# Performance work log

Measured on AMD Instinct MI355X. Metric: run time of the kernel, lower is better.

The kernel has to match this reference:

```python
import jax, jax.numpy as jnp
import numpy as np

B, D, M, R, C = 1024, 32, 8, 4096, 32
TOPK_P = 0.1  # hard-coded in torch forward
EPS = 1e-9


def setup_inputs() -> dict:
    key = jax.random.key(0)
    k0, k1, k2, k3, k4 = jax.random.split(key, 5)
    x = jax.random.normal(k0, (B, D), dtype=jnp.float32)
    centers = jax.random.normal(k1, (D, M), dtype=jnp.float32)
    # widths kept away from 0 so gaussian MFs don't all underflow
    widths = jax.random.uniform(k2, (D, M), dtype=jnp.float32, minval=0.5, maxval=1.5)
    consequents = jax.random.uniform(k3, (R, D + 1, C), dtype=jnp.float32)
    rules = jax.random.randint(k4, (R, D), 0, M, dtype=jnp.int32)
    return {"x": x, "centers": centers, "widths": widths,
            "consequents": consequents, "rules": rules}


def reference(x, centers, widths, consequents, rules):
    Bn, Dn = x.shape
    Rn = rules.shape[0]
    # Gaussian membership functions: (B, D, M)
    mfs = jnp.exp(-((x[:, :, None] - centers[None]) ** 2) / (2.0 * widths[None] ** 2))
    # Gather per-rule MF values: (B, D, R)  (torch.gather along mf axis)
    rule_mfs = mfs[:, jnp.arange(Dn)[:, None], rules.T]
    # Firing strengths via product over input dims: (B, R)
    firing = jnp.prod(rule_mfs, axis=1)
    # top-K gate + scatter mask
    K = max(1, int(TOPK_P * Rn))
    _, idx = jax.lax.top_k(firing, K)
    mask = jnp.zeros_like(firing).at[jnp.arange(Bn)[:, None], idx].set(1.0)
    firing = firing * mask
    norm_fs = firing / (firing.sum(axis=1, keepdims=True) + EPS)
    # zeroG=False branch. Torch does einsum('bi,rjc->brc', x_ext, consequents)
    # which sums i and j independently: rule_mfs[b,r,c] = sum_i(x_ext[b,i]) * sum_j(cons[r,j,c]).
    # Then einsum('br,brc->bc') => out = sum(x_ext,1) * (norm_fs @ sum(cons,1)).
    x_ext_sum = x.sum(axis=1) + 1.0          # sum over x_ext = [x, 1], shape (B,)
    cons_sum = consequents.sum(axis=1)       # (R, C)
    rule_outputs = x_ext_sum[:, None] * (norm_fs @ cons_sum)  # (B, C)
    return rule_outputs, norm_fs, mask
```

## Files before the change

kernel.cpp:

```cpp
#include <hip/hip_runtime.h>

#define Bn 1024
#define Dn 32
#define Mn 8
#define Rn 4096
#define Cn 32
#define Kn 409
#define NTH 512
#define NBIN 1024
#define CCAP 256

typedef unsigned int u32;
typedef unsigned short u16;
typedef short bf16x8 __attribute__((ext_vector_type(8)));
typedef float f32x4 __attribute__((ext_vector_type(4)));

__device__ __forceinline__ int binof(float kf) {
    int b = (int)floorf(kf * (float)(NBIN / 120.0) + (float)NBIN);
    return b < 0 ? 0 : (b > NBIN - 1 ? NBIN - 1 : b);
}

__device__ __forceinline__ u16 f2bf(float v) {
    u32 b = __float_as_uint(v);
    b += 0x7fffu + ((b >> 16) & 1u);
    return (u16)(b >> 16);
}

__device__ __forceinline__ uint4 onehot4(int v) {
    uint4 o;
    o.x = (v == 0 ? 0x3F80u : 0u) | (v == 1 ? (0x3F80u << 16) : 0u);
    o.y = (v == 2 ? 0x3F80u : 0u) | (v == 3 ? (0x3F80u << 16) : 0u);
    o.z = (v == 4 ? 0x3F80u : 0u) | (v == 5 ? (0x3F80u << 16) : 0u);
    o.w = (v == 6 ? 0x3F80u : 0u) | (v == 7 ? (0x3F80u << 16) : 0u);
    return o;
}

__global__ __launch_bounds__(NTH, 8) void key_gemm_kernel(
    const float* __restrict__ x, const float* __restrict__ centers,
    const float* __restrict__ widths, const float* __restrict__ cons,
    const int* __restrict__ rules,
    float* __restrict__ cons_sum, float* __restrict__ keys)
{
    __shared__ float s_cen[256];
    __shared__ float s_inv[256];
    __shared__ u16 sAh[32 * 32];
    __shared__ u16 sAl[32 * 32];
    __shared__ u16 sB[128 * 32];

    const int blk = blockIdx.x;
    const int t = threadIdx.x;
    const int lane = t & 63;
    const int w = t >> 6;
    const int m0 = (blk >> 5) * 32;
    const int n0 = (blk & 31) * 128;
    const int wr = w >> 2;
    const int wc = w & 3;

    if (t < 256) {
        const float ww = widths[t];
        s_cen[t] = centers[t];
        s_inv[t] = 0.5f / (ww * ww);
    }

    f32x4 acc0 = (f32x4){0.f, 0.f, 0.f, 0.f};
    f32x4 acc1 = (f32x4){0.f, 0.f, 0.f, 0.f};

    const int brow = t >> 2;
    const int aj = t & 3;
    const int cidx = blk * 128 + (t & 127);
    const float* cp = cons + (size_t)(cidx >> 5) * ((Dn + 1) * Cn) + (cidx & 31);
    float csum = 0.f;
    __syncthreads();

#pragma unroll
    for (int ki = 0; ki < 8; ++ki) {
        const int d0 = ki * 4;
        {
            const int v = rules[(size_t)(n0 + brow) * Dn + d0 + aj];
            *(uint4*)(sB + brow * 32 + aj * 8) = onehot4(v);
        }
        if (t < 128) {
            const int arow = t >> 2;
            const float xv = x[(size_t)(m0 + arow) * Dn + d0 + aj];
            const int dm0 = (d0 + aj) * 8;
            u16 h[8], l[8];
#pragma unroll
            for (int m = 0; m < 8; ++m) {
                const float dx = xv - s_cen[dm0 + m];
                const float e = -(dx * dx) * s_inv[dm0 + m];
                const u16 hb = f2bf(e);
                h[m] = hb;
                l[m] = f2bf(e - __uint_as_float((u32)hb << 16));
            }
            *(uint4*)(sAh + arow * 32 + aj * 8) =
                make_uint4((u32)h[0] | ((u32)h[1] << 16), (u32)h[2] | ((u32)h[3] << 16),
                           (u32)h[4] | ((u32)h[5] << 16), (u32)h[6] | ((u32)h[7] << 16));
            *(uint4*)(sAl + arow * 32 + aj * 8) =
                make_uint4((u32)l[0] | ((u32)l[1] << 16), (u32)l[2] | ((u32)l[3] << 16),
                           (u32)l[4] | ((u32)l[5] << 16), (u32)l[6] | ((u32)l[7] << 16));
#pragma unroll
            for (int q = 0; q < 4; ++q) csum += cp[(ki * 4 + q) * Cn];
        }
        __syncthreads();
        bf16x8 ah = *(const bf16x8*)(sAh + ((wr * 16 + (lane & 15)) * 32 + (lane >> 4) * 8));
        bf16x8 al = *(const bf16x8*)(sAl + ((wr * 16 + (lane & 15)) * 32 + (lane >> 4) * 8));
        bf16x8 b0 = *(const bf16x8*)(sB + ((wc * 32 + (lane & 15)) * 32 + (lane >> 4) * 8));
        bf16x8 b1 = *(const bf16x8*)(sB + ((wc * 32 + 16 + (lane & 15)) * 32 + (lane >> 4) * 8));
        acc0 = __builtin_amdgcn_mfma_f32_16x16x32_bf16(ah, b0, acc0, 0, 0, 0);
        acc0 = __builtin_amdgcn_mfma_f32_16x16x32_bf16(al, b0, acc0, 0, 0, 0);
        acc1 = __builtin_amdgcn_mfma_f32_16x16x32_bf16(ah, b1, acc1, 0, 0, 0);
        acc1 = __builtin_amdgcn_mfma_f32_16x16x32_bf16(al, b1, acc1, 0, 0, 0);
        __syncthreads();
    }
    if (t < 128) {
        csum += cp[Dn * Cn];
        cons_sum[cidx] = csum;
    }
    const int cr = (lane >> 4) * 4;
    const int cc = lane & 15;
#pragma unroll
    for (int reg = 0; reg < 4; ++reg) {
        keys[(size_t)(m0 + wr * 16 + cr + reg) * Rn + (n0 + wc * 32 + cc)] = acc0[reg];
        keys[(size_t)(m0 + wr * 16 + cr + reg) * Rn + (n0 + wc * 32 + 16 + cc)] = acc1[reg];
    }
}

__global__ __launch_bounds__(NTH, 8) void select_kernel(
    const float* __restrict__ x,
    const float* __restrict__ centers,
    const float* __restrict__ widths,
    const float* __restrict__ keys,
    const int* __restrict__ rules,
    const float* __restrict__ cons_sum,
    float* __restrict__ out_rule,
    float* __restrict__ out_norm,
    float* __restrict__ out_mask)
{
    __shared__ float  s_x[Dn];
    __shared__ double s_e[256];
    __shared__ u32    s_hist[NBIN + 2];
    __shared__ u32    s_selmask[Rn / 32];
    __shared__ int    s_wtot[8];
    __shared__ float  s_wsum[8];
    __shared__ int    s_wpre[8];
    __shared__ int    s_cidx[CCAP];
    __shared__ double s_cval[CCAP];
    __shared__ int    s_selidx[Kn + 8];
    __shared__ float  s_selv[Kn + 8];
    __shared__ float  s_red[NTH];
    __shared__ int    s_bb, s_ccnt;

    const int t = threadIdx.x;
    const int lane = t & 63;
    const int w = t >> 6;
    const int b = blockIdx.x;

    const f32x4* kptr = (const f32x4*)(keys + (size_t)b * Rn);
    f32x4 ka = kptr[t];
    f32x4 kb = kptr[NTH + t];

    if (t < Dn) s_x[t] = x[b * Dn + t];
    if (t == 0) { s_ccnt = 0; s_hist[NBIN] = 0u; s_hist[NBIN + 1] = 0u; }
    s_hist[t] = 0u;
    s_hist[t + NTH] = 0u;
    if (t < Rn / 32) s_selmask[t] = 0u;
    __syncthreads();

    if (t < 256) {
        const int d = t >> 3;
        const double dx = (double)s_x[d] - (double)centers[t];
        const double ww = (double)widths[t];
        s_e[t] = -(dx * dx) / (2.0 * (ww * ww));
    }
    atomicAdd(&s_hist[binof(ka.x)], 1u);
    atomicAdd(&s_hist[binof(ka.y)], 1u);
    atomicAdd(&s_hist[binof(ka.z)], 1u);
    atomicAdd(&s_hist[binof(ka.w)], 1u);
    atomicAdd(&s_hist[binof(kb.x)], 1u);
    atomicAdd(&s_hist[binof(kb.y)], 1u);
    atomicAdd(&s_hist[binof(kb.z)], 1u);
    atomicAdd(&s_hist[binof(kb.w)], 1u);
    __syncthreads();

    const int h0 = (int)s_hist[2 * t];
    const int h1 = (int)s_hist[2 * t + 1];
    const int loc = h0 + h1;
    int S = loc;
#pragma unroll
    for (int off = 1; off < 64; off <<= 1) {
        const int vv = __shfl(S, lane + off < 64 ? lane + off : lane);
        if (lane + off < 64) S += vv;
    }
    if (lane == 0) s_wtot[w] = S;
    __syncthreads();
    int wsuf = 0;
#pragma unroll
    for (int ww = 0; ww < 8; ++ww) wsuf += (ww > w) ? s_wtot[ww] : 0;
    const int full = S + wsuf;
    s_hist[2 * t] = (u32)full;
    s_hist[2 * t + 1] = (u32)(full - h0);
    if (full - loc < Kn && full >= Kn) {
        s_bb = (full - h0 >= Kn) ? (2 * t + 1) : (2 * t);
    }
    __syncthreads();
    const int bb = s_bb;
    const int hi = (bb + 1 > NBIN - 1) ? NBIN - 1 : bb + 1;
    const int lo = (bb - 1 < 0) ? 0 : bb - 1;
    const int Acnt = (int)s_hist[hi + 1];
    const int want_in = Kn - Acnt;

#define CAND(kf, ridx) { const int bn = binof(kf); \
        if (bn >= lo && bn <= hi) { const int pos = atomicAdd(&s_ccnt, 1); \
            if (pos < CCAP) s_cidx[pos] = (ridx); } }
    CAND(ka.x, 4 * t + 0) CAND(ka.y, 4 * t + 1) CAND(ka.z, 4 * t + 2) CAND(ka.w, 4 * t + 3)
    CAND(kb.x, 2048 + 4 * t + 0) CAND(kb.y, 2048 + 4 * t + 1)
    CAND(kb.z, 2048 + 4 * t + 2) CAND(kb.w, 2048 + 4 * t + 3)
#undef CAND
    __syncthreads();
    const int cnt = s_ccnt < CCAP ? s_ccnt : CCAP;
    if (t < cnt) {
        const int* rp = rules + s_cidx[t] * Dn;
        double s = 0.0;
#pragma unroll
        for (int d = 0; d < Dn; ++d) s += s_e[d * 8 + rp[d]];
        s_cval[t] = s;
    }
    __syncthreads();
    if (t < cnt) {
        const double mv = s_cval[t];
        const int mi = s_cidx[t];
        int rank = 0;
        for (int j = 0; j < cnt; ++j) {
            const double ov = s_cval[j];
            const int oi = s_cidx[j];
            rank += ((ov > mv) || (ov == mv && oi < mi)) ? 1 : 0;
        }
        if (rank < want_in) atomicOr(&s_selmask[mi >> 5], 1u << (mi & 31));
    }
    __syncthreads();

    u32 selbits = 0u;
    int cnt_sel = 0;
    float lsum = 0.f;
#define SEL(kf, ridx, bit) { const int bn = binof(kf); \
        bool sel = (bn > hi); \
        if (!sel && bn >= lo) sel = (s_selmask[(ridx) >> 5] >> ((ridx) & 31)) & 1u; \
        float f = 0.f; \
        if (sel) { f = expf(kf); selbits |= (1u << (bit)); ++cnt_sel; lsum += f; } \
        kf = f; }
    SEL(ka.x, 4 * t + 0, 0) SEL(ka.y, 4 * t + 1, 1) SEL(ka.z, 4 * t + 2, 2) SEL(ka.w, 4 * t + 3, 3)
    SEL(kb.x, 2048 + 4 * t + 0, 4) SEL(kb.y, 2048 + 4 * t + 1, 5)
    SEL(kb.z, 2048 + 4 * t + 2, 6) SEL(kb.w, 2048 + 4 * t + 3, 7)
#undef SEL
#pragma unroll
    for (int off = 32; off >= 1; off >>= 1) lsum += __shfl_xor(lsum, off);
    if (lane == 0) s_wsum[w] = lsum;
    int p = cnt_sel;
#pragma unroll
    for (int off = 1; off < 64; off <<= 1) {
        const int u = __shfl(p, lane >= off ? lane - off : lane);
        if (lane >= off) p += u;
    }
    if (lane == 63) s_wpre[w] = p;
    __syncthreads();
    float denom = 1e-9f;
#pragma unroll
    for (int ww = 0; ww < 8; ++ww) denom += s_wsum[ww];
    const float rinv = 1.0f / denom;
    int base = 0, nsel = 0;
#pragma unroll
    for (int ww = 0; ww < 8; ++ww) { base += (ww < w) ? s_wpre[ww] : 0; nsel += s_wpre[ww]; }
    int pos = base + (p - cnt_sel);

#define CPT(fv, ridx, bit) if ((selbits >> (bit)) & 1u) { s_selidx[pos] = (ridx); s_selv[pos] = fv; ++pos; }
    CPT(ka.x, 4 * t + 0, 0) CPT(ka.y, 4 * t + 1, 1) CPT(ka.z, 4 * t + 2, 2) CPT(ka.w, 4 * t + 3, 3)
    CPT(kb.x, 2048 + 4 * t + 0, 4) CPT(kb.y, 2048 + 4 * t + 1, 5)
    CPT(kb.z, 2048 + 4 * t + 2, 6) CPT(kb.w, 2048 + 4 * t + 3, 7)
#undef CPT

    {
        f32x4* onorm = (f32x4*)(out_norm + (size_t)b * Rn);
        f32x4* omask = (f32x4*)(out_mask + (size_t)b * Rn);
        f32x4 nv, mk;
        nv.x = ka.x * rinv; mk.x = (selbits & 1u) ? 1.f : 0.f;
        nv.y = ka.y * rinv; mk.y = (selbits & 2u) ? 1.f : 0.f;
        nv.z = ka.z * rinv; mk.z = (selbits & 4u) ? 1.f : 0.f;
        nv.w = ka.w * rinv; mk.w = (selbits & 8u) ? 1.f : 0.f;
        __builtin_nontemporal_store(nv, &onorm[t]);
        __builtin_nontemporal_store(mk, &omask[t]);
        nv.x = kb.x * rinv; mk.x = (selbits & 16u) ? 1.f : 0.f;
        nv.y = kb.y * rinv; mk.y = (selbits & 32u) ? 1.f : 0.f;
        nv.z = kb.z * rinv; mk.z = (selbits & 64u) ? 1.f : 0.f;
        nv.w = kb.w * rinv; mk.w = (selbits & 128u) ? 1.f : 0.f;
        __builtin_nontemporal_store(nv, &onorm[NTH + t]);
        __builtin_nontemporal_store(mk, &omask[NTH + t]);
    }
    __syncthreads();

    const int g = t >> 5;
    const int c = t & 31;
    float acc = 0.f;
    for (int i = g; i < nsel; i += 16) {
        acc += s_selv[i] * cons_sum[s_selidx[i] * Cn + c];
    }
    s_red[t] = acc;
    __syncthreads();
    if (t < Cn) {
        float ss = 0.f;
#pragma unroll
        for (int gg = 0; gg < 16; ++gg) ss += s_red[gg * 32 + t];
        float xs = 1.f;
#pragma unroll
        for (int d = 0; d < Dn; ++d) xs += s_x[d];
        __builtin_nontemporal_store(xs * ss * rinv, &out_rule[(size_t)b * Cn + t]);
    }
}

extern "C" void kernel_launch(void* const* d_in, const int* in_sizes, int n_in,
                              void* d_out, int out_size, void* d_ws, size_t ws_size,
                              hipStream_t stream) {
    (void)in_sizes; (void)n_in; (void)out_size; (void)ws_size;
    const float* x = (const float*)d_in[0];
    const float* centers = (const float*)d_in[1];
    const float* widths = (const float*)d_in[2];
    const float* consequents = (const float*)d_in[3];
    const int* rules = (const int*)d_in[4];

    float* out_rule = (float*)d_out;
    float* out_norm = out_rule + (size_t)Bn * Cn;
    float* out_mask = out_norm + (size_t)Bn * Rn;

    char* wsb = (char*)d_ws;
    float* cons_sum = (float*)wsb;
    float* keys = (float*)(wsb + (512 << 10));

    key_gemm_kernel<<<1024, NTH, 0, stream>>>(x, centers, widths, consequents, rules,
                                              cons_sum, keys);
    select_kernel<<<Bn, NTH, 0, stream>>>(x, centers, widths, keys, rules, cons_sum,
                                          out_rule, out_norm, out_mask);
}
```

Baseline: 43.90 us.

## Store GEMM keys as bf16 and recompute selected firing values exactly

The intermediate key matrix written by the GEMM kernel is now staged through shared memory, converted to bf16 and stored with coalesced 16-byte writes. This halves the workspace traffic between the two kernels. The select kernel widens the candidate bin margin to tolerate bf16 rounding. It then recomputes exact double-precision log-firing values only for the selected rules, via a rules gather, instead of exponentiating keys for every element. This trades an extra per-selected-rule gather loop and more syncs for less memory bandwidth, and depends on the wider margin and the candidate capacity being enough to keep top-k exact.

```diff
diff --git a/kernel.cpp b/kernel.cpp
--- a/kernel.cpp
+++ b/kernel.cpp
@@ -9,6 +9,7 @@
 #define NTH 512
 #define NBIN 1024
 #define CCAP 256
+#define MARG 4
 
 typedef unsigned int u32;
 typedef unsigned short u16;
@@ -39,7 +40,7 @@
     const float* __restrict__ x, const float* __restrict__ centers,
     const float* __restrict__ widths, const float* __restrict__ cons,
     const int* __restrict__ rules,
-    float* __restrict__ cons_sum, float* __restrict__ keys)
+    float* __restrict__ cons_sum, u16* __restrict__ keys)
 {
     __shared__ float s_cen[256];
     __shared__ float s_inv[256];
@@ -116,12 +117,19 @@
         csum += cp[Dn * Cn];
         cons_sum[cidx] = csum;
     }
-    const int cr = (lane >> 4) * 4;
-    const int cc = lane & 15;
-#pragma unroll
-    for (int reg = 0; reg < 4; ++reg) {
-        keys[(size_t)(m0 + wr * 16 + cr + reg) * Rn + (n0 + wc * 32 + cc)] = acc0[reg];
-        keys[(size_t)(m0 + wr * 16 + cr + reg) * Rn + (n0 + wc * 32 + 16 + cc)] = acc1[reg];
+    {
+        const int cr = (lane >> 4) * 4;
+        const int cc = lane & 15;
+#pragma unroll
+        for (int reg = 0; reg < 4; ++reg) {
+            const int row = wr * 16 + cr + reg;
+            sB[row * 128 + wc * 32 + cc] = f2bf(acc0[reg]);
+            sB[row * 128 + wc * 32 + 16 + cc] = f2bf(acc1[reg]);
+        }
+        __syncthreads();
+        const int row = t >> 4;
+        const int col0 = (t & 15) * 8;
+        *(uint4*)(keys + (size_t)(m0 + row) * Rn + n0 + col0) = *(const uint4*)(sB + row * 128 + col0);
     }
 }
 
@@ -129,7 +137,7 @@
     const float* __restrict__ x,
     const float* __restrict__ centers,
     const float* __restrict__ widths,
-    const float* __restrict__ keys,
+    const u16* __restrict__ keys,
     const int* __restrict__ rules,
     const float* __restrict__ cons_sum,
     float* __restrict__ out_rule,
@@ -155,9 +163,12 @@
     const int w = t >> 6;
     const int b = blockIdx.x;
 
-    const f32x4* kptr = (const f32x4*)(keys + (size_t)b * Rn);
-    f32x4 ka = kptr[t];
-    f32x4 kb = kptr[NTH + t];
+    const uint4 kv = ((const uint4*)(keys + (size_t)b * Rn))[t];
+    float k[8];
+    k[0] = __uint_as_float(kv.x << 16); k[1] = __uint_as_float(kv.x & 0xFFFF0000u);
+    k[2] = __uint_as_float(kv.y << 16); k[3] = __uint_as_float(kv.y & 0xFFFF0000u);
+    k[4] = __uint_as_float(kv.z << 16); k[5] = __uint_as_float(kv.z & 0xFFFF0000u);
+    k[6] = __uint_as_float(kv.w << 16); k[7] = __uint_as_float(kv.w & 0xFFFF0000u);
 
     if (t < Dn) s_x[t] = x[b * Dn + t];
     if (t == 0) { s_ccnt = 0; s_hist[NBIN] = 0u; s_hist[NBIN + 1] = 0u; }
@@ -172,14 +183,8 @@
         const double ww = (double)widths[t];
         s_e[t] = -(dx * dx) / (2.0 * (ww * ww));
     }
-    atomicAdd(&s_hist[binof(ka.x)], 1u);
-    atomicAdd(&s_hist[binof(ka.y)], 1u);
-    atomicAdd(&s_hist[binof(ka.z)], 1u);
-    atomicAdd(&s_hist[binof(ka.w)], 1u);
-    atomicAdd(&s_hist[binof(kb.x)], 1u);
-    atomicAdd(&s_hist[binof(kb.y)], 1u);
-    atomicAdd(&s_hist[binof(kb.z)], 1u);
-    atomicAdd(&s_hist[binof(kb.w)], 1u);
+#pragma unroll
+    for (int j = 0; j < 8; ++j) atomicAdd(&s_hist[binof(k[j])], 1u);
     __syncthreads();
 
     const int h0 = (int)s_hist[2 * t];
@@ -204,18 +209,19 @@
     }
     __syncthreads();
     const int bb = s_bb;
-    const int hi = (bb + 1 > NBIN - 1) ? NBIN - 1 : bb + 1;
-    const int lo = (bb - 1 < 0) ? 0 : bb - 1;
+    const int hi = (bb + MARG > NBIN - 1) ? NBIN - 1 : bb + MARG;
+    const int lo = (bb - MARG < 0) ? 0 : bb - MARG;
     const int Acnt = (int)s_hist[hi + 1];
     const int want_in = Kn - Acnt;
 
-#define CAND(kf, ridx) { const int bn = binof(kf); \
-        if (bn >= lo && bn <= hi) { const int pos = atomicAdd(&s_ccnt, 1); \
-            if (pos < CCAP) s_cidx[pos] = (ridx); } }
-    CAND(ka.x, 4 * t + 0) CAND(ka.y, 4 * t + 1) CAND(ka.z, 4 * t + 2) CAND(ka.w, 4 * t + 3)
-    CAND(kb.x, 2048 + 4 * t + 0) CAND(kb.y, 2048 + 4 * t + 1)
-    CAND(kb.z, 2048 + 4 * t + 2) CAND(kb.w, 2048 + 4 * t + 3)
-#undef CAND
+#pragma unroll
+    for (int j = 0; j < 8; ++j) {
+        const int bn = binof(k[j]);
+        if (bn >= lo && bn <= hi) {
+            const int pos = atomicAdd(&s_ccnt, 1);
+            if (pos < CCAP) s_cidx[pos] = 8 * t + j;
+        }
+    }
     __syncthreads();
     const int cnt = s_ccnt < CCAP ? s_ccnt : CCAP;
     if (t < cnt) {
@@ -241,20 +247,14 @@
 
     u32 selbits = 0u;
     int cnt_sel = 0;
-    float lsum = 0.f;
-#define SEL(kf, ridx, bit) { const int bn = binof(kf); \
-        bool sel = (bn > hi); \
-        if (!sel && bn >= lo) sel = (s_selmask[(ridx) >> 5] >> ((ridx) & 31)) & 1u; \
-        float f = 0.f; \
-        if (sel) { f = expf(kf); selbits |= (1u << (bit)); ++cnt_sel; lsum += f; } \
-        kf = f; }
-    SEL(ka.x, 4 * t + 0, 0) SEL(ka.y, 4 * t + 1, 1) SEL(ka.z, 4 * t + 2, 2) SEL(ka.w, 4 * t + 3, 3)
-    SEL(kb.x, 2048 + 4 * t + 0, 4) SEL(kb.y, 2048 + 4 * t + 1, 5)
-    SEL(kb.z, 2048 + 4 * t + 2, 6) SEL(kb.w, 2048 + 4 * t + 3, 7)
-#undef SEL
-#pragma unroll
-    for (int off = 32; off >= 1; off >>= 1) lsum += __shfl_xor(lsum, off);
-    if (lane == 0) s_wsum[w] = lsum;
+#pragma unroll
+    for (int j = 0; j < 8; ++j) {
+        const int bn = binof(k[j]);
+        const int r = 8 * t + j;
+        bool sel = (bn > hi);
+        if (!sel && bn >= lo) sel = (s_selmask[r >> 5] >> (r & 31)) & 1u;
+        if (sel) { selbits |= (1u << j); ++cnt_sel; }
+    }
     int p = cnt_sel;
 #pragma unroll
     for (int off = 1; off < 64; off <<= 1) {
@@ -263,37 +263,55 @@
     }
     if (lane == 63) s_wpre[w] = p;
     __syncthreads();
+    int base = 0, nsel = 0;
+#pragma unroll
+    for (int ww = 0; ww < 8; ++ww) { base += (ww < w) ? s_wpre[ww] : 0; nsel += s_wpre[ww]; }
+    int pos = base + (p - cnt_sel);
+    const int mypos0 = pos;
+#pragma unroll
+    for (int j = 0; j < 8; ++j) {
+        if ((selbits >> j) & 1u) s_selidx[pos++] = 8 * t + j;
+    }
+    __syncthreads();
+
+    if (t < nsel) {
+        const int* rp = rules + s_selidx[t] * Dn;
+        double s = 0.0;
+#pragma unroll
+        for (int d = 0; d < Dn; ++d) s += s_e[d * 8 + rp[d]];
+        s_selv[t] = expf((float)s);
+    }
+    __syncthreads();
+    float lsum = (t < nsel) ? s_selv[t] : 0.f;
+#pragma unroll
+    for (int off = 32; off >= 1; off >>= 1) lsum += __shfl_xor(lsum, off);
+    if (lane == 0) s_wsum[w] = lsum;
+    __syncthreads();
     float denom = 1e-9f;
 #pragma unroll
     for (int ww = 0; ww < 8; ++ww) denom += s_wsum[ww];
     const float rinv = 1.0f / denom;
-    int base = 0, nsel = 0;
-#pragma unroll
-    for (int ww = 0; ww < 8; ++ww) { base += (ww < w) ? s_wpre[ww] : 0; nsel += s_wpre[ww]; }
-    int pos = base + (p - cnt_sel);
-
-#define CPT(fv, ridx, bit) if ((selbits >> (bit)) & 1u) { s_selidx[pos] = (ridx); s_selv[pos] = fv; ++pos; }
-    CPT(ka.x, 4 * t + 0, 0) CPT(ka.y, 4 * t + 1, 1) CPT(ka.z, 4 * t + 2, 2) CPT(ka.w, 4 * t + 3, 3)
-    CPT(kb.x, 2048 + 4 * t + 0, 4) CPT(kb.y, 2048 + 4 * t + 1, 5)
-    CPT(kb.z, 2048 + 4 * t + 2, 6) CPT(kb.w, 2048 + 4 * t + 3, 7)
-#undef CPT
 
     {
+        f32x4 nv0, nv1, mk0, mk1;
+        int rp2 = mypos0;
+        float v[8];
+#pragma unroll
+        for (int j = 0; j < 8; ++j) {
+            v[j] = ((selbits >> j) & 1u) ? s_selv[rp2++] * rinv : 0.f;
+        }
+        nv0.x = v[0]; nv0.y = v[1]; nv0.z = v[2]; nv0.w = v[3];
+        nv1.x = v[4]; nv1.y = v[5]; nv1.z = v[6]; nv1.w = v[7];
+        mk0.x = (selbits & 1u) ? 1.f : 0.f;  mk0.y = (selbits & 2u) ? 1.f : 0.f;
+        mk0.z = (selbits & 4u) ? 1.f : 0.f;  mk0.w = (selbits & 8u) ? 1.f : 0.f;
+        mk1.x = (selbits & 16u) ? 1.f : 0.f; mk1.y = (selbits & 32u) ? 1.f : 0.f;
+        mk1.z = (selbits & 64u) ? 1.f : 0.f; mk1.w = (selbits & 128u) ? 1.f : 0.f;
         f32x4* onorm = (f32x4*)(out_norm + (size_t)b * Rn);
         f32x4* omask = (f32x4*)(out_mask + (size_t)b * Rn);
-        f32x4 nv, mk;
-        nv.x = ka.x * rinv; mk.x = (selbits & 1u) ? 1.f : 0.f;
-        nv.y = ka.y * rinv; mk.y = (selbits & 2u) ? 1.f : 0.f;
-        nv.z = ka.z * rinv; mk.z = (selbits & 4u) ? 1.f : 0.f;
-        nv.w = ka.w * rinv; mk.w = (selbits & 8u) ? 1.f : 0.f;
-        __builtin_nontemporal_store(nv, &onorm[t]);
-        __builtin_nontemporal_store(mk, &omask[t]);
-        nv.x = kb.x * rinv; mk.x = (selbits & 16u) ? 1.f : 0.f;
-        nv.y = kb.y * rinv; mk.y = (selbits & 32u) ? 1.f : 0.f;
-        nv.z = kb.z * rinv; mk.z = (selbits & 64u) ? 1.f : 0.f;
-        nv.w = kb.w * rinv; mk.w = (selbits & 128u) ? 1.f : 0.f;
-        __builtin_nontemporal_store(nv, &onorm[NTH + t]);
-        __builtin_nontemporal_store(mk, &omask[NTH + t]);
+        __builtin_nontemporal_store(nv0, &onorm[2 * t]);
+        __builtin_nontemporal_store(nv1, &onorm[2 * t + 1]);
+        __builtin_nontemporal_store(mk0, &omask[2 * t]);
+        __builtin_nontemporal_store(mk1, &omask[2 * t + 1]);
     }
     __syncthreads();
 
@@ -332,7 +350,7 @@
 
     char* wsb = (char*)d_ws;
     float* cons_sum = (float*)wsb;
-    float* keys = (float*)(wsb + (512 << 10));
+    u16*   keys = (u16*)(wsb + (512 << 10));
 
     key_gemm_kernel<<<1024, NTH, 0, stream>>>(x, centers, widths, consequents, rules,
                                               cons_sum, keys);
```

Result: slower. 53.38 us (+21.6%).
